# Kernel optimization log

Measured on AMD Instinct MI355X. Metric: run time of the kernel, lower is better.

The kernel has to match this reference:

```python
import jax, jax.numpy as jnp
import numpy as np

T, V, L, N, D = 4, 2, 3, 4000, 256
TEMP = 0.5


def setup_inputs() -> dict:
    key = jax.random.key(0)
    ks = jax.random.split(key, 9)
    E = jax.random.normal(ks[0], (T, V, L, N, D), dtype=jnp.float32)
    s = 1.0 / np.sqrt(D)
    W1 = jax.random.uniform(ks[1], (D, D), jnp.float32, -s, s)
    b1 = jax.random.uniform(ks[2], (D,), jnp.float32, -s, s)
    W2 = jax.random.uniform(ks[3], (D, D), jnp.float32, -s, s)
    b2 = jax.random.uniform(ks[4], (D,), jnp.float32, -s, s)
    idx_prio = jax.random.randint(ks[5], (2, V, L, 100), 0, N, dtype=jnp.int32)
    idx_rest = jax.random.randint(ks[6], (2, V, L, 20), 0, N, dtype=jnp.int32)
    neg_idx_prio = jax.random.randint(ks[7], (2, V, L, 3, 50), 0, N, dtype=jnp.int32)
    neg_idx_rest = jax.random.randint(ks[8], (2, V, L, 3, 10), 0, N, dtype=jnp.int32)
    return {
        "node_embeddings": E, "W1": W1, "b1": b1, "W2": W2, "b2": b2,
        "idx_prio": idx_prio, "idx_rest": idx_rest,
        "neg_idx_prio": neg_idx_prio, "neg_idx_rest": neg_idx_rest,
        "num_views": 2, "num_layers": 3,
    }


def _proj_norm(x, W1, b1, W2, b2):
    # nn.Linear -> ReLU -> nn.Linear, then F.normalize(p=2, dim=-1)
    h = jax.nn.relu(x @ W1.T + b1)
    z = h @ W2.T + b2
    return z / jnp.maximum(jnp.linalg.norm(z, axis=-1, keepdims=True), 1e-12)


def _type_loss(P, t, idx, nidx):
    # P: [T,V,L,N,D] projected+normalized; idx: [V,L,S] anchor node ids;
    # nidx: [V,L,3,K] cross-type negative node ids (one row per other type).
    vi = jnp.arange(V)[:, None, None]
    li = jnp.arange(L)[None, :, None]
    z = P[t][vi, li, idx]                                  # [V,L,S,D] anchors
    # positives: same node index across every other (view, layer) combo
    Pj = P[t][:, :, idx, :]                                # [X,Y,V,L,S,D]
    sims_pos = jnp.einsum('vlsd,xyvlsd->vlsxy', z, Pj) / TEMP
    same_vl = (jnp.eye(V, dtype=bool)[:, None, :, None]
               & jnp.eye(L, dtype=bool)[None, :, None, :])  # [V,L,X,Y]
    pos = jnp.where(same_vl[:, :, None, :, :], 0.0,
                    jnp.exp(sims_pos)).sum((-2, -1))        # [V,L,S]
    # within-type negatives: the other sampled anchors at the same (v,l)
    S = idx.shape[-1]
    sims_in = jnp.einsum('vlsd,vltd->vlst', z, z) / TEMP
    neg_in = jnp.where(jnp.eye(S, dtype=bool), 0.0,
                       jnp.exp(sims_in)).sum(-1)            # [V,L,S]
    # cross-type negatives: K sampled nodes from each other type at (v,l)
    others = jnp.array([o for o in range(T) if o != t])
    Po = P[others]                                          # [3,V,L,N,D]
    nidx2 = jnp.moveaxis(nidx, 2, 0)                        # [3,V,L,K]
    Pneg = jnp.take_along_axis(Po, nidx2[..., None], axis=3)  # [3,V,L,K,D]
    sims_c = jnp.einsum('vlsd,ovlkd->vlsok', z, Pneg) / TEMP
    neg = neg_in + jnp.exp(sims_c).sum((-2, -1))            # [V,L,S]
    loss = -jnp.log(pos / (pos + neg))
    return loss.sum(), loss.size


def reference(node_embeddings, W1, b1, W2, b2, idx_prio, idx_rest,
              neg_idx_prio, neg_idx_rest, num_views, num_layers):
    P = _proj_norm(node_embeddings, W1, b1, W2, b2)  # [T,V,L,N,D]
    total = jnp.float32(0.0)
    count = 0
    for t in range(T):  # small fixed loop over node types
        if t < 2:
            ls, c = _type_loss(P, t, idx_prio[t], neg_idx_prio[t])
        else:
            ls, c = _type_loss(P, t, idx_rest[t - 2], neg_idx_rest[t - 2])
        total = total + ls
        count += c
    return total / count
```

## Files before the change

kernel.cpp:

```cpp
#include <hip/hip_runtime.h>
#include <math.h>

#define DD 256
#define NV 2
#define NL 3
#define NNODE 4000
#define NROWS_B 8640
#define NROWS 10800
#define ACC_OFF (10800L * 256)
#define NANCH 1440
#define WP_OFF (ACC_OFF + 2 * NANCH)
#define XPAD 260

typedef __attribute__((ext_vector_type(8))) short short8;
typedef __attribute__((ext_vector_type(4))) short short4v;
typedef __attribute__((ext_vector_type(4))) float f32x4;

__device__ __forceinline__ unsigned short f2bf(float f) {
  unsigned u = __float_as_uint(f);
  u += 0x7fff + ((u >> 16) & 1);
  return (unsigned short)(u >> 16);
}

__device__ __forceinline__ int tb_B(int t) { return (t < 2) ? t * 3600 : 7200 + (t - 2) * 720; }
__device__ __forceinline__ int tb_C(int t) { return (t < 2) ? t * 900 : 1800 + (t - 2) * 180; }
__device__ __forceinline__ int anch_base(int t, int vl) {
  return ((t < 2) ? t * 600 : 1200 + (t - 2) * 120) + vl * ((t < 2) ? 100 : 20);
}
__device__ __forceinline__ int zrow_id(int t, int v, int l, int s, int S) {
  int vl = v * NL + l;
  return tb_B(t) + ((vl * NV + v) * NL + l) * S + s;
}

__device__ __forceinline__ long row_src(int u, const int* __restrict__ ip,
                                        const int* __restrict__ ir,
                                        const int* __restrict__ npg,
                                        const int* __restrict__ nrg) {
  int t, x, y, node;
  if (u < NROWS_B) {
    int S, u2;
    if (u < 7200) { t = u / 3600; u2 = u - t * 3600; S = 100; }
    else { int w = u - 7200; t = 2 + w / 720; u2 = w % 720; S = 20; }
    int s = u2 % S; int t1 = u2 / S;
    int l = t1 % NL; int t2 = t1 / NL;
    int v = t2 % NV; int xy = t2 / NV;
    x = xy / NL; y = xy % NL;
    if (t < 2) node = ip[((t * NV + v) * NL + l) * 100 + s];
    else       node = ir[(((t - 2) * NV + v) * NL + l) * 20 + s];
  } else {
    int w = u - NROWS_B;
    int K, u2;
    if (w < 1800) { t = w / 900; u2 = w % 900; K = 50; }
    else { int w2 = w - 1800; t = 2 + w2 / 180; u2 = w2 % 180; K = 10; }
    int k = u2 % K; int t1 = u2 / K;
    int l = t1 % NL; int t2 = t1 / NL;
    int v = t2 % NV; int o = t2 / NV;
    if (t < 2) node = npg[(((t * NV + v) * NL + l) * 3 + o) * 50 + k];
    else       node = nrg[((((t - 2) * NV + v) * NL + l) * 3 + o) * 10 + k];
    int ot = (o < t) ? o : o + 1;
    t = ot; x = v; y = l;
  }
  return ((((long)t * NV + x) * NL + y) * NNODE + node) * DD;
}

__global__ __launch_bounds__(256) void k_prep(const float* __restrict__ W1,
                                              const float* __restrict__ W2,
                                              float* __restrict__ ws) {
  int tid = blockIdx.x * 256 + threadIdx.x;
  if (tid < 2 * NANCH) ws[ACC_OFF + tid] = 0.0f;
  int st = tid >> 13, rem = tid & 8191;
  int cg = rem >> 9, kstep = (rem >> 6) & 7, lane = rem & 63;
  const float* W = st ? W2 : W1;
  int col = cg * 16 + (lane & 15);
  int k0 = kstep * 32 + (lane >> 4) * 8;
  unsigned short v[8] __attribute__((aligned(16)));
#pragma unroll
  for (int j = 0; j < 8; ++j) v[j] = f2bf(W[col * DD + k0 + j]);
  unsigned short* wp = (unsigned short*)(ws + WP_OFF);
  *(uint4*)(wp + (long)tid * 8) = *(const uint4*)v;
}

__global__ __launch_bounds__(256) void k_proj(const float* __restrict__ E,
                                              const float* __restrict__ b1,
                                              const float* __restrict__ b2,
                                              const int* __restrict__ ip,
                                              const int* __restrict__ ir,
                                              const int* __restrict__ npg,
                                              const int* __restrict__ nrg,
                                              float* __restrict__ ws) {
  __shared__ unsigned short Xs[32][XPAD];
  __shared__ unsigned short Hs[32][XPAD];
  __shared__ float ssbuf[2][32];
  const int tid = threadIdx.x;
  const int u0 = blockIdx.x * 32;
  const int wv = tid >> 6, l64 = tid & 63;
  const int quad = l64 >> 4, l15 = l64 & 15;
  const int rhalf = wv & 1, chalf = wv >> 1;
  const int rb = rhalf * 16, cb = chalf * 128;
  const unsigned short* wp = (const unsigned short*)(ws + WP_OFF);

  for (int i = 0; i < 8; ++i) {
    int r = wv * 8 + i;
    int u = u0 + r;
    float4 val = make_float4(0.f, 0.f, 0.f, 0.f);
    if (u < NROWS) {
      long src = row_src(u, ip, ir, npg, nrg);
      val = *(const float4*)(E + src + l64 * 4);
    }
    unsigned short h[4] __attribute__((aligned(8)));
    h[0] = f2bf(val.x); h[1] = f2bf(val.y); h[2] = f2bf(val.z); h[3] = f2bf(val.w);
    *(uint2*)(&Xs[r][l64 * 4]) = *(const uint2*)h;
  }

  f32x4 acc[8];
#pragma unroll
  for (int cg = 0; cg < 8; ++cg) {
    float bv = b1[cb + cg * 16 + l15];
    acc[cg] = (f32x4){bv, bv, bv, bv};
  }
  __syncthreads();
#pragma unroll
  for (int ks = 0; ks < 8; ++ks) {
    const unsigned short* ap = &Xs[rb + l15][ks * 32 + quad * 8];
    short4v alo = *(const short4v*)(ap);
    short4v ahi = *(const short4v*)(ap + 4);
    short8 a = __builtin_shufflevector(alo, ahi, 0, 1, 2, 3, 4, 5, 6, 7);
#pragma unroll
    for (int cg = 0; cg < 8; ++cg) {
      short8 b = *(const short8*)(wp + ((long)(((chalf * 8 + cg) * 8 + ks) * 64 + l64)) * 8);
      acc[cg] = __builtin_amdgcn_mfma_f32_16x16x32_bf16(a, b, acc[cg], 0, 0, 0);
    }
  }
#pragma unroll
  for (int cg = 0; cg < 8; ++cg) {
    int col = cb + cg * 16 + l15;
#pragma unroll
    for (int reg = 0; reg < 4; ++reg) {
      int row = rb + quad * 4 + reg;
      Hs[row][col] = f2bf(fmaxf(acc[cg][reg], 0.0f));
    }
  }
#pragma unroll
  for (int cg = 0; cg < 8; ++cg) {
    float bv = b2[cb + cg * 16 + l15];
    acc[cg] = (f32x4){bv, bv, bv, bv};
  }
  __syncthreads();
#pragma unroll
  for (int ks = 0; ks < 8; ++ks) {
    const unsigned short* ap = &Hs[rb + l15][ks * 32 + quad * 8];
    short4v alo = *(const short4v*)(ap);
    short4v ahi = *(const short4v*)(ap + 4);
    short8 a = __builtin_shufflevector(alo, ahi, 0, 1, 2, 3, 4, 5, 6, 7);
#pragma unroll
    for (int cg = 0; cg < 8; ++cg) {
      short8 b = *(const short8*)(wp + ((long)((16 + chalf * 8 + cg) * 8 + ks) * 64 + l64) * 8);
      acc[cg] = __builtin_amdgcn_mfma_f32_16x16x32_bf16(a, b, acc[cg], 0, 0, 0);
    }
  }
  float ss[4];
#pragma unroll
  for (int reg = 0; reg < 4; ++reg) {
    float s = 0.f;
#pragma unroll
    for (int cg = 0; cg < 8; ++cg) s = fmaf(acc[cg][reg], acc[cg][reg], s);
    ss[reg] = s;
  }
#pragma unroll
  for (int m = 1; m < 16; m <<= 1) {
#pragma unroll
    for (int reg = 0; reg < 4; ++reg) ss[reg] += __shfl_xor(ss[reg], m, 64);
  }
  if (l15 == 0) {
#pragma unroll
    for (int reg = 0; reg < 4; ++reg) ssbuf[chalf][rb + quad * 4 + reg] = ss[reg];
  }
  __syncthreads();
#pragma unroll
  for (int reg = 0; reg < 4; ++reg) {
    int row = rb + quad * 4 + reg;
    int u = u0 + row;
    if (u < NROWS) {
      float tot = ssbuf[0][row] + ssbuf[1][row];
      float sc = 1.0f / fmaxf(sqrtf(tot), 1e-12f);
#pragma unroll
      for (int cg = 0; cg < 8; ++cg)
        ws[(long)u * DD + cb + cg * 16 + l15] = acc[cg][reg] * sc;
    }
  }
}

__global__ __launch_bounds__(256) void k_pos(float* __restrict__ ws) {
  const int b = blockIdx.x;
  const int t = b / 36, r = b % 36, vl = r / 6, xy = r % 6;
  if (xy == vl) return;
  const int v = vl / NL, l = vl % NL;
  const int S = (t < 2) ? 100 : 20;
  const int tid = threadIdx.x;
  const int sub = tid & 3;
  const int ab = anch_base(t, vl);
  for (int s0 = 0; s0 < S; s0 += 64) {
    int s = s0 + (tid >> 2);
    if (s >= S) break;
    const float4* za = (const float4*)(ws + (long)zrow_id(t, v, l, s, S) * DD);
    const float4* pa = (const float4*)(ws + (long)(tb_B(t) + ((xy * NV + v) * NL + l) * S + s) * DD);
    float d = 0.0f;
#pragma unroll
    for (int i = 0; i < 16; ++i) {
      float4 a = za[sub + 4 * i];
      float4 bb = pa[sub + 4 * i];
      d = fmaf(a.x, bb.x, d); d = fmaf(a.y, bb.y, d);
      d = fmaf(a.z, bb.z, d); d = fmaf(a.w, bb.w, d);
    }
    d += __shfl_xor(d, 1, 4);
    d += __shfl_xor(d, 2, 4);
    if (sub == 0) atomicAdd(&ws[ACC_OFF + ab + s], expf(2.0f * d));
  }
}

#define ZPAD2 260
__global__ __launch_bounds__(256) void k_neg(float* __restrict__ ws) {
  __shared__ float Zt[64][ZPAD2];
  __shared__ float Pt[32][ZPAD2];
  const int b = blockIdx.x;
  int t, vl, c, A0, A;
  if (b < 192) { t = b / 96; int r = b % 96; vl = r / 16; int w = r % 16;
                 A0 = (w / 8) * 50; A = 50; c = w % 8; }
  else { int q = b - 192; t = 2 + q / 18; int r2 = q % 18; vl = r2 / 3;
         c = r2 % 3; A0 = 0; A = 20; }
  const int v = vl / NL, l = vl % NL;
  const int S = (t < 2) ? 100 : 20, K = (t < 2) ? 50 : 10;
  const int Ptot = S + 3 * K;
  const int q0 = c * 32;
  const int pn = min(32, Ptot - q0);
  const int tid = threadIdx.x;
  const int tx = tid & 15, ty = tid >> 4;

  for (int e = tid; e < A * 64; e += 256) {
    int a = e >> 6, kk = (e & 63) * 4;
    long zr = (long)zrow_id(t, v, l, A0 + a, S) * DD;
    *(float4*)(&Zt[a][kk]) = *(const float4*)(ws + zr + kk);
  }
  for (int e = tid; e < pn * 64; e += 256) {
    int p = e >> 6, kk = (e & 63) * 4;
    int qg = q0 + p;
    long row;
    if (qg < S) row = zrow_id(t, v, l, qg, S);
    else { int q2 = qg - S; int o = q2 / K, k2 = q2 % K;
           row = NROWS_B + tb_C(t) + ((o * NV + v) * NL + l) * K + k2; }
    *(float4*)(&Pt[p][kk]) = *(const float4*)(ws + row * DD + kk);
  }
  __syncthreads();

  float acc[4][2];
#pragma unroll
  for (int i = 0; i < 4; ++i) { acc[i][0] = 0.f; acc[i][1] = 0.f; }

  for (int k0 = 0; k0 < DD; k0 += 8) {
    float4 zr0[4], zr1[4];
#pragma unroll
    for (int i = 0; i < 4; ++i) {
      zr0[i] = *(const float4*)(&Zt[ty + 16 * i][k0]);
      zr1[i] = *(const float4*)(&Zt[ty + 16 * i][k0 + 4]);
    }
#pragma unroll
    for (int j = 0; j < 2; ++j) {
      float4 p0 = *(const float4*)(&Pt[tx + 16 * j][k0]);
      float4 p1 = *(const float4*)(&Pt[tx + 16 * j][k0 + 4]);
#pragma unroll
      for (int i = 0; i < 4; ++i) {
        float s = acc[i][j];
        s = fmaf(zr0[i].x, p0.x, s); s = fmaf(zr0[i].y, p0.y, s);
        s = fmaf(zr0[i].z, p0.z, s); s = fmaf(zr0[i].w, p0.w, s);
        s = fmaf(zr1[i].x, p1.x, s); s = fmaf(zr1[i].y, p1.y, s);
        s = fmaf(zr1[i].z, p1.z, s); s = fmaf(zr1[i].w, p1.w, s);
        acc[i][j] = s;
      }
    }
  }

#pragma unroll
  for (int i = 0; i < 4; ++i) {
    int a = ty + 16 * i;
    float sum = 0.0f;
    if (a < A) {
      int sg = A0 + a;
#pragma unroll
      for (int j = 0; j < 2; ++j) {
        int qg = q0 + tx + 16 * j;
        if (qg < Ptot && !(qg < S && qg == sg)) sum += expf(2.0f * acc[i][j]);
      }
    }
    for (int o = 8; o > 0; o >>= 1) sum += __shfl_xor(sum, o, 16);
    if (a < A && tx == 0)
      atomicAdd(&ws[ACC_OFF + NANCH + anch_base(t, vl) + A0 + a], sum);
  }
}

__global__ __launch_bounds__(256) void k_fin(const float* __restrict__ ws,
                                             float* __restrict__ out) {
  __shared__ float red[256];
  const int tid = threadIdx.x;
  float sum = 0.0f;
  for (int i = tid; i < NANCH; i += 256) {
    float p = ws[ACC_OFF + i];
    float n = ws[ACC_OFF + NANCH + i];
    sum += -logf(p / (p + n));
  }
  red[tid] = sum;
  __syncthreads();
  for (int s = 128; s > 0; s >>= 1) {
    if (tid < s) red[tid] += red[tid + s];
    __syncthreads();
  }
  if (tid == 0) out[0] = red[0] / (float)NANCH;
}

extern "C" void kernel_launch(void* const* d_in, const int* in_sizes, int n_in,
                              void* d_out, int out_size, void* d_ws, size_t ws_size,
                              hipStream_t stream) {
  const float* E  = (const float*)d_in[0];
  const float* W1 = (const float*)d_in[1];
  const float* b1 = (const float*)d_in[2];
  const float* W2 = (const float*)d_in[3];
  const float* b2 = (const float*)d_in[4];
  const int* ip  = (const int*)d_in[5];
  const int* ir  = (const int*)d_in[6];
  const int* npg = (const int*)d_in[7];
  const int* nrg = (const int*)d_in[8];
  float* ws = (float*)d_ws;
  float* out = (float*)d_out;

  hipLaunchKernelGGL(k_prep, dim3(64), dim3(256), 0, stream, W1, W2, ws);
  hipLaunchKernelGGL(k_proj, dim3((NROWS + 31) / 32), dim3(256), 0, stream,
                     E, b1, b2, ip, ir, npg, nrg, ws);
  hipLaunchKernelGGL(k_pos, dim3(144), dim3(256), 0, stream, ws);
  hipLaunchKernelGGL(k_neg, dim3(228), dim3(256), 0, stream, ws);
  hipLaunchKernelGGL(k_fin, dim3(1), dim3(256), 0, stream, ws, out);
}
```

Before: 204.3 us.

## Fuse positive/negative/final kernels into one bf16 MFMA similarity kernel

Stores projected rows as bf16 and replaces the separate positive-dot, negative-GEMM and final-reduction kernels with a single kernel. It computes all anchor-versus-candidate similarities with bf16 MFMA, extracting positives from the diagonal. A last-block atomic counter performs the final log-loss reduction. This removes two launches and halves intermediate traffic, but computes many off-diagonal positive-block products that are then discarded, and lowers precision of the similarities.

```diff
diff --git a/kernel.cpp b/kernel.cpp
--- a/kernel.cpp
+++ b/kernel.cpp
@@ -7,10 +7,12 @@
 #define NNODE 4000
 #define NROWS_B 8640
 #define NROWS 10800
-#define ACC_OFF (10800L * 256)
 #define NANCH 1440
-#define WP_OFF (ACC_OFF + 2 * NANCH)
+#define ACC_OFF (10800L * 128)
+#define CNT_IDX (ACC_OFF + 2 * NANCH)
+#define WP_OFF (ACC_OFF + 2 * NANCH + 4)
 #define XPAD 260
+#define NBLK_SIM 96
 
 typedef __attribute__((ext_vector_type(8))) short short8;
 typedef __attribute__((ext_vector_type(4))) short short4v;
@@ -26,10 +28,6 @@
 __device__ __forceinline__ int tb_C(int t) { return (t < 2) ? t * 900 : 1800 + (t - 2) * 180; }
 __device__ __forceinline__ int anch_base(int t, int vl) {
   return ((t < 2) ? t * 600 : 1200 + (t - 2) * 120) + vl * ((t < 2) ? 100 : 20);
-}
-__device__ __forceinline__ int zrow_id(int t, int v, int l, int s, int S) {
-  int vl = v * NL + l;
-  return tb_B(t) + ((vl * NV + v) * NL + l) * S + s;
 }
 
 __device__ __forceinline__ long row_src(int u, const int* __restrict__ ip,
@@ -67,7 +65,7 @@
                                               const float* __restrict__ W2,
                                               float* __restrict__ ws) {
   int tid = blockIdx.x * 256 + threadIdx.x;
-  if (tid < 2 * NANCH) ws[ACC_OFF + tid] = 0.0f;
+  if (tid < 2 * NANCH + 4) ws[ACC_OFF + tid] = 0.0f;
   int st = tid >> 13, rem = tid & 8191;
   int cg = rem >> 9, kstep = (rem >> 6) & 7, lane = rem & 63;
   const float* W = st ? W2 : W1;
@@ -98,6 +96,7 @@
   const int rhalf = wv & 1, chalf = wv >> 1;
   const int rb = rhalf * 16, cb = chalf * 128;
   const unsigned short* wp = (const unsigned short*)(ws + WP_OFF);
+  unsigned short* zb = (unsigned short*)ws;
 
   for (int i = 0; i < 8; ++i) {
     int r = wv * 8 + i;
@@ -185,135 +184,112 @@
       float sc = 1.0f / fmaxf(sqrtf(tot), 1e-12f);
 #pragma unroll
       for (int cg = 0; cg < 8; ++cg)
-        ws[(long)u * DD + cb + cg * 16 + l15] = acc[cg][reg] * sc;
-    }
-  }
-}
-
-__global__ __launch_bounds__(256) void k_pos(float* __restrict__ ws) {
+        zb[(long)u * DD + cb + cg * 16 + l15] = f2bf(acc[cg][reg] * sc);
+    }
+  }
+}
+
+__global__ __launch_bounds__(256) void k_sim(float* __restrict__ ws,
+                                             float* __restrict__ out) {
+  __shared__ float negL[112];
+  __shared__ float red[256];
+  __shared__ int lastFlag;
+  const unsigned short* zb = (const unsigned short*)ws;
+  float* posG = ws + ACC_OFF;
+  float* negG = ws + ACC_OFF + NANCH;
+  int* cnt = (int*)(ws + CNT_IDX);
+
   const int b = blockIdx.x;
-  const int t = b / 36, r = b % 36, vl = r / 6, xy = r % 6;
-  if (xy == vl) return;
-  const int v = vl / NL, l = vl % NL;
-  const int S = (t < 2) ? 100 : 20;
-  const int tid = threadIdx.x;
-  const int sub = tid & 3;
-  const int ab = anch_base(t, vl);
-  for (int s0 = 0; s0 < S; s0 += 64) {
-    int s = s0 + (tid >> 2);
-    if (s >= S) break;
-    const float4* za = (const float4*)(ws + (long)zrow_id(t, v, l, s, S) * DD);
-    const float4* pa = (const float4*)(ws + (long)(tb_B(t) + ((xy * NV + v) * NL + l) * S + s) * DD);
-    float d = 0.0f;
-#pragma unroll
-    for (int i = 0; i < 16; ++i) {
-      float4 a = za[sub + 4 * i];
-      float4 bb = pa[sub + 4 * i];
-      d = fmaf(a.x, bb.x, d); d = fmaf(a.y, bb.y, d);
-      d = fmaf(a.z, bb.z, d); d = fmaf(a.w, bb.w, d);
-    }
-    d += __shfl_xor(d, 1, 4);
-    d += __shfl_xor(d, 2, 4);
-    if (sub == 0) atomicAdd(&ws[ACC_OFF + ab + s], expf(2.0f * d));
-  }
-}
-
-#define ZPAD2 260
-__global__ __launch_bounds__(256) void k_neg(float* __restrict__ ws) {
-  __shared__ float Zt[64][ZPAD2];
-  __shared__ float Pt[32][ZPAD2];
-  const int b = blockIdx.x;
-  int t, vl, c, A0, A;
-  if (b < 192) { t = b / 96; int r = b % 96; vl = r / 16; int w = r % 16;
-                 A0 = (w / 8) * 50; A = 50; c = w % 8; }
-  else { int q = b - 192; t = 2 + q / 18; int r2 = q % 18; vl = r2 / 3;
-         c = r2 % 3; A0 = 0; A = 20; }
+  int t, vl, c;
+  if (b < 72) { t = b / 36; int r = b % 36; vl = r / 6; c = r % 6; }
+  else { int q = b - 72; t = 2 + q / 12; int r2 = q % 12; vl = r2 / 2; c = r2 % 2; }
   const int v = vl / NL, l = vl % NL;
   const int S = (t < 2) ? 100 : 20, K = (t < 2) ? 50 : 10;
-  const int Ptot = S + 3 * K;
-  const int q0 = c * 32;
-  const int pn = min(32, Ptot - q0);
+  const int Ptot = 6 * S + 3 * K;
+  const int q0 = c * 128;
+  const int rem = Ptot - q0;
+  const int NT = ((rem < 128 ? rem : 128) + 15) / 16;
+  const int MT = (S + 15) / 16;
   const int tid = threadIdx.x;
-  const int tx = tid & 15, ty = tid >> 4;
-
-  for (int e = tid; e < A * 64; e += 256) {
-    int a = e >> 6, kk = (e & 63) * 4;
-    long zr = (long)zrow_id(t, v, l, A0 + a, S) * DD;
-    *(float4*)(&Zt[a][kk]) = *(const float4*)(ws + zr + kk);
-  }
-  for (int e = tid; e < pn * 64; e += 256) {
-    int p = e >> 6, kk = (e & 63) * 4;
-    int qg = q0 + p;
-    long row;
-    if (qg < S) row = zrow_id(t, v, l, qg, S);
-    else { int q2 = qg - S; int o = q2 / K, k2 = q2 % K;
-           row = NROWS_B + tb_C(t) + ((o * NV + v) * NL + l) * K + k2; }
-    *(float4*)(&Pt[p][kk]) = *(const float4*)(ws + row * DD + kk);
-  }
-  __syncthreads();
-
-  float acc[4][2];
-#pragma unroll
-  for (int i = 0; i < 4; ++i) { acc[i][0] = 0.f; acc[i][1] = 0.f; }
-
-  for (int k0 = 0; k0 < DD; k0 += 8) {
-    float4 zr0[4], zr1[4];
-#pragma unroll
-    for (int i = 0; i < 4; ++i) {
-      zr0[i] = *(const float4*)(&Zt[ty + 16 * i][k0]);
-      zr1[i] = *(const float4*)(&Zt[ty + 16 * i][k0 + 4]);
-    }
-#pragma unroll
-    for (int j = 0; j < 2; ++j) {
-      float4 p0 = *(const float4*)(&Pt[tx + 16 * j][k0]);
-      float4 p1 = *(const float4*)(&Pt[tx + 16 * j][k0 + 4]);
-#pragma unroll
-      for (int i = 0; i < 4; ++i) {
-        float s = acc[i][j];
-        s = fmaf(zr0[i].x, p0.x, s); s = fmaf(zr0[i].y, p0.y, s);
-        s = fmaf(zr0[i].z, p0.z, s); s = fmaf(zr0[i].w, p0.w, s);
-        s = fmaf(zr1[i].x, p1.x, s); s = fmaf(zr1[i].y, p1.y, s);
-        s = fmaf(zr1[i].z, p1.z, s); s = fmaf(zr1[i].w, p1.w, s);
-        acc[i][j] = s;
+  const int wv = tid >> 6, l64 = tid & 63;
+  const int quad = l64 >> 4, l15 = l64 & 15;
+  const int ab = anch_base(t, vl);
+  const int rowZbase = tb_B(t) + ((vl * NV + v) * NL + l) * S;
+
+  for (int mt = wv; mt < MT; mt += 4) {
+    int am = mt * 16 + l15;
+    int amc = (am < S) ? am : (S - 1);
+    const unsigned short* abase = zb + (long)(rowZbase + amc) * DD + quad * 8;
+    short8 afr[8];
+#pragma unroll
+    for (int ks = 0; ks < 8; ++ks) afr[ks] = *(const short8*)(abase + ks * 32);
+    float negAcc[4] = {0.f, 0.f, 0.f, 0.f};
+    for (int nt = 0; nt < NT; ++nt) {
+      int qg = q0 + nt * 16 + l15;
+      bool vq = (qg < Ptot);
+      int qc = vq ? qg : 0;
+      int rowb, xy = -1, j = -1;
+      if (qc < 6 * S) {
+        xy = qc / S; j = qc - xy * S;
+        rowb = tb_B(t) + ((xy * NV + v) * NL + l) * S + j;
+      } else {
+        int q2 = qc - 6 * S; int o = q2 / K, k2 = q2 - o * K;
+        rowb = NROWS_B + tb_C(t) + ((o * NV + v) * NL + l) * K + k2;
       }
-    }
-  }
-
-#pragma unroll
-  for (int i = 0; i < 4; ++i) {
-    int a = ty + 16 * i;
-    float sum = 0.0f;
-    if (a < A) {
-      int sg = A0 + a;
-#pragma unroll
-      for (int j = 0; j < 2; ++j) {
-        int qg = q0 + tx + 16 * j;
-        if (qg < Ptot && !(qg < S && qg == sg)) sum += expf(2.0f * acc[i][j]);
+      const unsigned short* bbase = zb + (long)rowb * DD + quad * 8;
+      f32x4 acc = {0.f, 0.f, 0.f, 0.f};
+#pragma unroll
+      for (int ks = 0; ks < 8; ++ks) {
+        short8 bfr = *(const short8*)(bbase + ks * 32);
+        acc = __builtin_amdgcn_mfma_f32_16x16x32_bf16(afr[ks], bfr, acc, 0, 0, 0);
       }
-    }
-    for (int o = 8; o > 0; o >>= 1) sum += __shfl_xor(sum, o, 16);
-    if (a < A && tx == 0)
-      atomicAdd(&ws[ACC_OFF + NANCH + anch_base(t, vl) + A0 + a], sum);
-  }
-}
-
-__global__ __launch_bounds__(256) void k_fin(const float* __restrict__ ws,
-                                             float* __restrict__ out) {
-  __shared__ float red[256];
-  const int tid = threadIdx.x;
-  float sum = 0.0f;
-  for (int i = tid; i < NANCH; i += 256) {
-    float p = ws[ACC_OFF + i];
-    float n = ws[ACC_OFF + NANCH + i];
-    sum += -logf(p / (p + n));
-  }
-  red[tid] = sum;
-  __syncthreads();
-  for (int s = 128; s > 0; s >>= 1) {
-    if (tid < s) red[tid] += red[tid + s];
+#pragma unroll
+      for (int r = 0; r < 4; ++r) {
+        int a = mt * 16 + quad * 4 + r;
+        if (!vq || a >= S) continue;
+        float e = expf(2.0f * acc[r]);
+        if (xy >= 0) {
+          if (xy == vl) { if (j != a) negAcc[r] += e; }
+          else if (j == a) atomicAdd(&posG[ab + a], e);
+        } else {
+          negAcc[r] += e;
+        }
+      }
+    }
+#pragma unroll
+    for (int m = 1; m < 16; m <<= 1) {
+#pragma unroll
+      for (int r = 0; r < 4; ++r) negAcc[r] += __shfl_xor(negAcc[r], m, 64);
+    }
+    if (l15 == 0) {
+#pragma unroll
+      for (int r = 0; r < 4; ++r) negL[mt * 16 + quad * 4 + r] = negAcc[r];
+    }
+  }
+  __syncthreads();
+  for (int a = tid; a < S; a += 256) atomicAdd(&negG[ab + a], negL[a]);
+  __threadfence();
+  __syncthreads();
+  if (tid == 0) {
+    int old = atomicAdd(cnt, 1);
+    lastFlag = (old == NBLK_SIM - 1) ? 1 : 0;
+  }
+  __syncthreads();
+  if (lastFlag) {
+    float sum = 0.f;
+    for (int i = tid; i < NANCH; i += 256) {
+      float p = atomicAdd(&posG[i], 0.0f);
+      float n = atomicAdd(&negG[i], 0.0f);
+      sum += -logf(p / (p + n));
+    }
+    red[tid] = sum;
     __syncthreads();
-  }
-  if (tid == 0) out[0] = red[0] / (float)NANCH;
+    for (int s = 128; s > 0; s >>= 1) {
+      if (tid < s) red[tid] += red[tid + s];
+      __syncthreads();
+    }
+    if (tid == 0) out[0] = red[0] / (float)NANCH;
+  }
 }
 
 extern "C" void kernel_launch(void* const* d_in, const int* in_sizes, int n_in,
@@ -334,7 +310,5 @@
   hipLaunchKernelGGL(k_prep, dim3(64), dim3(256), 0, stream, W1, W2, ws);
   hipLaunchKernelGGL(k_proj, dim3((NROWS + 31) / 32), dim3(256), 0, stream,
                      E, b1, b2, ip, ir, npg, nrg, ws);
-  hipLaunchKernelGGL(k_pos, dim3(144), dim3(256), 0, stream, ws);
-  hipLaunchKernelGGL(k_neg, dim3(228), dim3(256), 0, stream, ws);
-  hipLaunchKernelGGL(k_fin, dim3(1), dim3(256), 0, stream, ws, out);
-}
+  hipLaunchKernelGGL(k_sim, dim3(NBLK_SIM), dim3(256), 0, stream, ws, out);
+}
```

Result: slower. 214.9 us (+5.2%).

## Restructure projection kernel as persistent 512-thread blocks with register-resident weights

Applied to the files above, without the earlier changes.

The projection kernel now launches 225 persistent blocks of 512 threads. Each block loops over three 16-row tiles and each wave owns 32 output columns. The bf16 weight fragments for both layers are loaded once into registers per wave and reused across tiles, so they are no longer re-read from global memory for every MFMA. The weight prepack layout is reordered to match, and LDS padding is changed so the A fragments load as single 16-byte vectors. The trade-offs are high register pressure from holding 32 short8 fragments, more barriers per tile, and a row count hard-coded to divide exactly (225*3*16 = 10800), with no bounds check.

```diff
diff --git a/kernel.cpp b/kernel.cpp
--- a/kernel.cpp
+++ b/kernel.cpp
@@ -7,13 +7,14 @@
 #define NNODE 4000
 #define NROWS_B 8640
 #define NROWS 10800
+#define NANCH 1440
 #define ACC_OFF (10800L * 256)
-#define NANCH 1440
-#define WP_OFF (ACC_OFF + 2 * NANCH)
-#define XPAD 260
+#define CNT_IDX (ACC_OFF + 2 * NANCH)
+#define WP_OFF (CNT_IDX + 4)
+#define XPAD 264
+#define NBLK_PROJ 225
 
 typedef __attribute__((ext_vector_type(8))) short short8;
-typedef __attribute__((ext_vector_type(4))) short short4v;
 typedef __attribute__((ext_vector_type(4))) float f32x4;
 
 __device__ __forceinline__ unsigned short f2bf(float f) {
@@ -67,12 +68,11 @@
                                               const float* __restrict__ W2,
                                               float* __restrict__ ws) {
   int tid = blockIdx.x * 256 + threadIdx.x;
-  if (tid < 2 * NANCH) ws[ACC_OFF + tid] = 0.0f;
-  int st = tid >> 13, rem = tid & 8191;
-  int cg = rem >> 9, kstep = (rem >> 6) & 7, lane = rem & 63;
+  if (tid < 2 * NANCH + 4) ws[ACC_OFF + tid] = 0.0f;
+  int st = tid >> 13, ks = (tid >> 10) & 7, cgg = (tid >> 6) & 15, lane = tid & 63;
   const float* W = st ? W2 : W1;
-  int col = cg * 16 + (lane & 15);
-  int k0 = kstep * 32 + (lane >> 4) * 8;
+  int col = cgg * 16 + (lane & 15);
+  int k0 = ks * 32 + (lane >> 4) * 8;
   unsigned short v[8] __attribute__((aligned(16)));
 #pragma unroll
   for (int j = 0; j < 8; ++j) v[j] = f2bf(W[col * DD + k0 + j]);
@@ -80,113 +80,110 @@
   *(uint4*)(wp + (long)tid * 8) = *(const uint4*)v;
 }
 
-__global__ __launch_bounds__(256) void k_proj(const float* __restrict__ E,
-                                              const float* __restrict__ b1,
-                                              const float* __restrict__ b2,
-                                              const int* __restrict__ ip,
-                                              const int* __restrict__ ir,
-                                              const int* __restrict__ npg,
-                                              const int* __restrict__ nrg,
-                                              float* __restrict__ ws) {
-  __shared__ unsigned short Xs[32][XPAD];
-  __shared__ unsigned short Hs[32][XPAD];
-  __shared__ float ssbuf[2][32];
+__global__ __launch_bounds__(512, 2) void k_proj(const float* __restrict__ E,
+                                                 const float* __restrict__ b1,
+                                                 const float* __restrict__ b2,
+                                                 const int* __restrict__ ip,
+                                                 const int* __restrict__ ir,
+                                                 const int* __restrict__ npg,
+                                                 const int* __restrict__ nrg,
+                                                 float* __restrict__ ws) {
+  __shared__ unsigned short Xs[16][XPAD];
+  __shared__ unsigned short Hs[16][XPAD];
+  __shared__ float ssbuf[8][16];
   const int tid = threadIdx.x;
-  const int u0 = blockIdx.x * 32;
   const int wv = tid >> 6, l64 = tid & 63;
   const int quad = l64 >> 4, l15 = l64 & 15;
-  const int rhalf = wv & 1, chalf = wv >> 1;
-  const int rb = rhalf * 16, cb = chalf * 128;
+  const int cb = wv * 32;
   const unsigned short* wp = (const unsigned short*)(ws + WP_OFF);
 
-  for (int i = 0; i < 8; ++i) {
-    int r = wv * 8 + i;
-    int u = u0 + r;
-    float4 val = make_float4(0.f, 0.f, 0.f, 0.f);
-    if (u < NROWS) {
-      long src = row_src(u, ip, ir, npg, nrg);
-      val = *(const float4*)(E + src + l64 * 4);
-    }
-    unsigned short h[4] __attribute__((aligned(8)));
-    h[0] = f2bf(val.x); h[1] = f2bf(val.y); h[2] = f2bf(val.z); h[3] = f2bf(val.w);
-    *(uint2*)(&Xs[r][l64 * 4]) = *(const uint2*)h;
-  }
-
-  f32x4 acc[8];
-#pragma unroll
-  for (int cg = 0; cg < 8; ++cg) {
-    float bv = b1[cb + cg * 16 + l15];
-    acc[cg] = (f32x4){bv, bv, bv, bv};
-  }
-  __syncthreads();
-#pragma unroll
-  for (int ks = 0; ks < 8; ++ks) {
-    const unsigned short* ap = &Xs[rb + l15][ks * 32 + quad * 8];
-    short4v alo = *(const short4v*)(ap);
-    short4v ahi = *(const short4v*)(ap + 4);
-    short8 a = __builtin_shufflevector(alo, ahi, 0, 1, 2, 3, 4, 5, 6, 7);
-#pragma unroll
-    for (int cg = 0; cg < 8; ++cg) {
-      short8 b = *(const short8*)(wp + ((long)(((chalf * 8 + cg) * 8 + ks) * 64 + l64)) * 8);
-      acc[cg] = __builtin_amdgcn_mfma_f32_16x16x32_bf16(a, b, acc[cg], 0, 0, 0);
-    }
-  }
-#pragma unroll
-  for (int cg = 0; cg < 8; ++cg) {
-    int col = cb + cg * 16 + l15;
+  short8 bfr[2][8][2];
+#pragma unroll
+  for (int st = 0; st < 2; ++st)
+#pragma unroll
+    for (int ks = 0; ks < 8; ++ks)
+#pragma unroll
+      for (int cg = 0; cg < 2; ++cg)
+        bfr[st][ks][cg] = *(const short8*)(
+            wp + ((long)(((st * 8 + ks) * 16 + (wv * 2 + cg)) * 64 + l64)) * 8);
+
+  float bv1[2], bv2[2];
+#pragma unroll
+  for (int cg = 0; cg < 2; ++cg) {
+    bv1[cg] = b1[cb + cg * 16 + l15];
+    bv2[cg] = b2[cb + cg * 16 + l15];
+  }
+
+  for (int it = 0; it < 3; ++it) {
+    int rt = blockIdx.x + it * NBLK_PROJ;
+    int u0 = rt * 16;
+
+#pragma unroll
+    for (int i = 0; i < 2; ++i) {
+      int r = wv * 2 + i;
+      long src = row_src(u0 + r, ip, ir, npg, nrg);
+      float4 val = *(const float4*)(E + src + l64 * 4);
+      unsigned short h[4] __attribute__((aligned(8)));
+      h[0] = f2bf(val.x); h[1] = f2bf(val.y); h[2] = f2bf(val.z); h[3] = f2bf(val.w);
+      *(uint2*)(&Xs[r][l64 * 4]) = *(const uint2*)h;
+    }
+    __syncthreads();
+
+    f32x4 acc[2];
+#pragma unroll
+    for (int cg = 0; cg < 2; ++cg) acc[cg] = (f32x4){bv1[cg], bv1[cg], bv1[cg], bv1[cg]};
+#pragma unroll
+    for (int ks = 0; ks < 8; ++ks) {
+      short8 a = *(const short8*)(&Xs[l15][ks * 32 + quad * 8]);
+#pragma unroll
+      for (int cg = 0; cg < 2; ++cg)
+        acc[cg] = __builtin_amdgcn_mfma_f32_16x16x32_bf16(a, bfr[0][ks][cg], acc[cg], 0, 0, 0);
+    }
+#pragma unroll
+    for (int cg = 0; cg < 2; ++cg) {
+      int col = cb + cg * 16 + l15;
+#pragma unroll
+      for (int reg = 0; reg < 4; ++reg)
+        Hs[quad * 4 + reg][col] = f2bf(fmaxf(acc[cg][reg], 0.0f));
+    }
+    __syncthreads();
+
+#pragma unroll
+    for (int cg = 0; cg < 2; ++cg) acc[cg] = (f32x4){bv2[cg], bv2[cg], bv2[cg], bv2[cg]};
+#pragma unroll
+    for (int ks = 0; ks < 8; ++ks) {
+      short8 a = *(const short8*)(&Hs[l15][ks * 32 + quad * 8]);
+#pragma unroll
+      for (int cg = 0; cg < 2; ++cg)
+        acc[cg] = __builtin_amdgcn_mfma_f32_16x16x32_bf16(a, bfr[1][ks][cg], acc[cg], 0, 0, 0);
+    }
+
+    float ss[4];
+#pragma unroll
+    for (int reg = 0; reg < 4; ++reg)
+      ss[reg] = fmaf(acc[0][reg], acc[0][reg], acc[1][reg] * acc[1][reg]);
+#pragma unroll
+    for (int m = 1; m < 16; m <<= 1) {
+#pragma unroll
+      for (int reg = 0; reg < 4; ++reg) ss[reg] += __shfl_xor(ss[reg], m, 64);
+    }
+    if (l15 == 0) {
+#pragma unroll
+      for (int reg = 0; reg < 4; ++reg) ssbuf[wv][quad * 4 + reg] = ss[reg];
+    }
+    __syncthreads();
 #pragma unroll
     for (int reg = 0; reg < 4; ++reg) {
-      int row = rb + quad * 4 + reg;
-      Hs[row][col] = f2bf(fmaxf(acc[cg][reg], 0.0f));
-    }
-  }
-#pragma unroll
-  for (int cg = 0; cg < 8; ++cg) {
-    float bv = b2[cb + cg * 16 + l15];
-    acc[cg] = (f32x4){bv, bv, bv, bv};
-  }
-  __syncthreads();
-#pragma unroll
-  for (int ks = 0; ks < 8; ++ks) {
-    const unsigned short* ap = &Hs[rb + l15][ks * 32 + quad * 8];
-    short4v alo = *(const short4v*)(ap);
-    short4v ahi = *(const short4v*)(ap + 4);
-    short8 a = __builtin_shufflevector(alo, ahi, 0, 1, 2, 3, 4, 5, 6, 7);
-#pragma unroll
-    for (int cg = 0; cg < 8; ++cg) {
-      short8 b = *(const short8*)(wp + ((long)((16 + chalf * 8 + cg) * 8 + ks) * 64 + l64) * 8);
-      acc[cg] = __builtin_amdgcn_mfma_f32_16x16x32_bf16(a, b, acc[cg], 0, 0, 0);
-    }
-  }
-  float ss[4];
-#pragma unroll
-  for (int reg = 0; reg < 4; ++reg) {
-    float s = 0.f;
-#pragma unroll
-    for (int cg = 0; cg < 8; ++cg) s = fmaf(acc[cg][reg], acc[cg][reg], s);
-    ss[reg] = s;
-  }
-#pragma unroll
-  for (int m = 1; m < 16; m <<= 1) {
-#pragma unroll
-    for (int reg = 0; reg < 4; ++reg) ss[reg] += __shfl_xor(ss[reg], m, 64);
-  }
-  if (l15 == 0) {
-#pragma unroll
-    for (int reg = 0; reg < 4; ++reg) ssbuf[chalf][rb + quad * 4 + reg] = ss[reg];
-  }
-  __syncthreads();
-#pragma unroll
-  for (int reg = 0; reg < 4; ++reg) {
-    int row = rb + quad * 4 + reg;
-    int u = u0 + row;
-    if (u < NROWS) {
-      float tot = ssbuf[0][row] + ssbuf[1][row];
+      int row = quad * 4 + reg;
+      float tot = 0.f;
+#pragma unroll
+      for (int w2 = 0; w2 < 8; ++w2) tot += ssbuf[w2][row];
       float sc = 1.0f / fmaxf(sqrtf(tot), 1e-12f);
 #pragma unroll
-      for (int cg = 0; cg < 8; ++cg)
-        ws[(long)u * DD + cb + cg * 16 + l15] = acc[cg][reg] * sc;
-    }
+      for (int cg = 0; cg < 2; ++cg)
+        ws[(long)(u0 + row) * DD + cb + cg * 16 + l15] = acc[cg][reg] * sc;
+    }
+    __syncthreads();
   }
 }
 
@@ -332,7 +329,7 @@
   float* out = (float*)d_out;
 
   hipLaunchKernelGGL(k_prep, dim3(64), dim3(256), 0, stream, W1, W2, ws);
-  hipLaunchKernelGGL(k_proj, dim3((NROWS + 31) / 32), dim3(256), 0, stream,
+  hipLaunchKernelGGL(k_proj, dim3(NBLK_PROJ), dim3(512), 0, stream,
                      E, b1, b2, ip, ir, npg, nrg, ws);
   hipLaunchKernelGGL(k_pos, dim3(144), dim3(256), 0, stream, ws);
   hipLaunchKernelGGL(k_neg, dim3(228), dim3(256), 0, stream, ws);
```

After: 180.9 us. -11.5%, faster.
